# Optimization experiments

Measured on AMD Instinct MI355X. Metric: run time of the kernel, lower is better.

The kernel has to match this reference:

```python
import jax, jax.numpy as jnp
import numpy as np

# ---- single-qubit gate matrices (theta may be scalar or batched (N,)) ----

def _rx(theta):
    t = theta * 0.5
    c = jnp.cos(t).astype(jnp.complex64)
    s = jnp.sin(t).astype(jnp.complex64)
    return jnp.stack([jnp.stack([c, -1j * s], -1), jnp.stack([-1j * s, c], -1)], -2)

def _ry(theta):
    t = theta * 0.5
    c = jnp.cos(t).astype(jnp.complex64)
    s = jnp.sin(t).astype(jnp.complex64)
    return jnp.stack([jnp.stack([c, -s], -1), jnp.stack([s, c], -1)], -2)

def _rz(theta):
    t = theta * 0.5
    e = jnp.exp(-1j * t.astype(jnp.complex64))
    z = jnp.zeros_like(e)
    return jnp.stack([jnp.stack([e, z], -1), jnp.stack([z, jnp.conj(e)], -1)], -2)

def _apply_1q(state, U, wire):
    # state: (N, 2^P) complex; U: (2,2) shared or (N,2,2) per-sample
    N = state.shape[0]
    s = state.reshape(N, 2 ** wire, 2, -1)
    if U.ndim == 3:
        s = jnp.einsum('nab,nxby->nxay', U, s)
    else:
        s = jnp.einsum('ab,nxby->nxay', U, s)
    return s.reshape(N, -1)

def _apply_cnot(state, c, t, P):
    # flip target axis where control bit == 1
    N = state.shape[0]
    s = state.reshape((N,) + (2,) * P)
    ac, at = 1 + c, 1 + t
    s0 = jnp.take(s, 0, axis=ac)
    s1 = jnp.take(s, 1, axis=ac)
    at2 = at if at < ac else at - 1
    s1 = jnp.flip(s1, axis=at2)
    s = jnp.stack([s0, s1], axis=ac)
    return s.reshape(N, -1)

def _circuit(angles, qweights, P):
    # angles: (N, P, 3); qweights: (L, P, 3) -> expvals (N, P)
    N = angles.shape[0]
    state = jnp.zeros((N, 2 ** P), jnp.complex64).at[:, 0].set(1.0)
    for i in range(P):  # encoding rotations (per-sample)
        state = _apply_1q(state, _rx(angles[:, i, 0]), i)
        state = _apply_1q(state, _ry(angles[:, i, 1]), i)
        state = _apply_1q(state, _rz(angles[:, i, 2]), i)
    for L in range(qweights.shape[0]):  # variational layers (shared weights)
        for i in range(P):
            state = _apply_1q(state, _ry(qweights[L, i, 0]), i)
            state = _apply_1q(state, _rz(qweights[L, i, 1]), i)
            state = _apply_1q(state, _ry(qweights[L, i, 2]), i)
        for i in range(P):  # ring CNOTs
            state = _apply_cnot(state, i, (i + 1) % P, P)
    probs = jnp.real(state * jnp.conj(state))  # (N, 2^P)
    idx = jnp.arange(2 ** P)
    bits = (idx[None, :] >> (P - 1 - jnp.arange(P))[:, None]) & 1  # wire 0 = MSB
    signs = (1 - 2 * bits).astype(jnp.float32)  # (P, 2^P)
    return probs @ signs.T  # <Z_i> per wire, (N, P)

def setup_inputs() -> dict:
    key = jax.random.key(0)
    ks = jax.random.split(key, 6)
    B, T, P, D, L = 2, 128, 13, 64, 2
    h = jax.random.normal(ks[0], (B, T, P, D), jnp.float32)
    enc_w = jax.random.normal(ks[1], (3, D), jnp.float32) * (1.0 / np.sqrt(D))
    enc_b = jax.random.normal(ks[2], (3,), jnp.float32) * 0.1
    qweights = jax.random.normal(ks[3], (L, P, 3), jnp.float32)
    dec_w = jax.random.normal(ks[4], (D, 1), jnp.float32) * 0.1
    alpha = jnp.full((1,), 0.05, jnp.float32)
    return {"h": h, "enc_w": enc_w, "enc_b": enc_b, "qweights": qweights, "dec_w": dec_w, "alpha": alpha}

def reference(h, enc_w, enc_b, qweights, dec_w, alpha):
    B, T, P, D = h.shape
    # encoder: Linear(D, 3)
    angles = (jnp.einsum('btpd,ad->btpa', h, enc_w) + enc_b).reshape(B * T, P, 3)
    expvals = _circuit(angles, qweights, P)  # (B*T, P)
    # decoder: Linear(1, D, bias=False)
    decoded = (expvals[:, :, None] * dec_w[:, 0][None, None, :]).reshape(B, T, P, D)
    return h + alpha[0] * decoded
```

## Files before the change

### kernel.cpp

```cpp
#include <hip/hip_runtime.h>

#define P   13
#define BLK 512
#define NH  (P * 64)

typedef float2 c2;

__device__ __forceinline__ c2 cmul2(c2 a, c2 b) {
    return make_float2(a.x * b.x - a.y * b.y, a.x * b.y + a.y * b.x);
}
__device__ __forceinline__ c2 cfma2(c2 a, c2 b, c2 c) {
    return make_float2(fmaf(a.x, b.x, fmaf(-a.y, b.y, c.x)),
                       fmaf(a.x, b.y, fmaf( a.y, b.x, c.y)));
}
__device__ __forceinline__ c2 shflx2(c2 v, int m) {
    c2 r; r.x = __shfl_xor(v.x, m, 64); r.y = __shfl_xor(v.y, m, 64); return r;
}

struct RowSet { unsigned r[13]; };
constexpr RowSet chain_rows(RowSet f) {
    for (int i = 0; i < 13; ++i) { int bc = 12 - i; int bt = (i == 12) ? 12 : (11 - i); f.r[bt] ^= f.r[bc]; }
    return f;
}
constexpr RowSet chain_cols(RowSet g) {
    for (int i = 0; i < 13; ++i) { int bc = 12 - i; int bt = (i == 12) ? 12 : (11 - i); g.r[bc] ^= g.r[bt]; }
    return g;
}
constexpr RowSet R0c {{0x0C00,0x0801,0x0003,0x0006,0x000C,0x0018,0x0030,0x0060,0x00C0,0x0180,0x0300,0x1600,0x1400}};
constexpr RowSet G0c {{0x1400,0x1C00,0x1C01,0x1C03,0x1C07,0x1C0F,0x1C1F,0x1C3F,0x1C7F,0x1CFF,0x1DFF,0x1FFF,0x0FFF}};
constexpr RowSet F1c = chain_rows(R0c);
constexpr RowSet F2c = chain_rows(F1c);
constexpr RowSet G1c = chain_cols(G0c);
static_assert(G1c.r[0]==0x0400 && G1c.r[1]==0x0800 && G1c.r[2]==0x0001 && G1c.r[3]==0x0002 &&
              G1c.r[4]==0x0004 && G1c.r[5]==0x0008 && G1c.r[6]==0x0010 && G1c.r[7]==0x0020 &&
              G1c.r[8]==0x0040 && G1c.r[9]==0x0080 && G1c.r[10]==0x0100 && G1c.r[11]==0x0200 &&
              G1c.r[12]==0x1000, "single-bit gate masks after chain 1");
static_assert(F1c.r[0]==0x0400 && F1c.r[1]==0x0800 && F1c.r[2]==0x0001 && F1c.r[12]==0x1000,
              "frame after chain 1 is the bit-permutation phi");

__device__ __forceinline__ void build_V(float wa, float wb, float wc, c2* u) {
    float a = 0.5f * wa, b = 0.5f * wb, c = 0.5f * wc;
    float sa, ca, sb, cb, sc, cc;
    __sincosf(a, &sa, &ca); __sincosf(b, &sb, &cb); __sincosf(c, &sc, &cc);
    float A = ca * cb, Bq = ca * sb, C = sa * cb, D = sa * sb;
    u[0] = make_float2( cc * A - sc * C, -cc * Bq - sc * D);
    u[1] = make_float2(-cc * C - sc * A,  cc * D - sc * Bq);
    u[2] = make_float2( sc * A + cc * C, -sc * Bq + cc * D);
    u[3] = make_float2(-sc * C + cc * A,  sc * D + cc * Bq);
}

template<int K>
__device__ __forceinline__ void gate_reg(c2* s, const float* m) {
    c2 u00 = {m[0], m[1]}, u01 = {m[2], m[3]}, u10 = {m[4], m[5]}, u11 = {m[6], m[7]};
#pragma unroll
    for (int r = 0; r < 16; ++r)
        if (!(r & (1 << K))) {
            const int r1 = r | (1 << K);
            c2 a0 = s[r], a1 = s[r1];
            s[r]  = cfma2(u00, a0, cmul2(u01, a1));
            s[r1] = cfma2(u10, a0, cmul2(u11, a1));
        }
}
template<int LM>
__device__ __forceinline__ void gate_lane(c2* s, const float* m, int lane) {
    c2 u00 = {m[0], m[1]}, u01 = {m[2], m[3]}, u10 = {m[4], m[5]}, u11 = {m[6], m[7]};
    int mb = (lane & LM) ? 1 : 0;
    c2 ua = mb ? u11 : u00, ub = mb ? u10 : u01;
#pragma unroll
    for (int r = 0; r < 16; ++r) {
        c2 pv = shflx2(s[r], LM);
        s[r] = cfma2(ua, s[r], cmul2(ub, pv));
    }
}

__global__ __launch_bounds__(BLK) void qlc_kernel(
    const float* __restrict__ h, const float* __restrict__ enc_w,
    const float* __restrict__ enc_b, const float* __restrict__ qw,
    const float* __restrict__ dec_w, const float* __restrict__ alpha,
    float* __restrict__ out, int nlayers)
{
    const int n = blockIdx.x, tid = threadIdx.x, lane = tid & 63, wv = tid >> 6;
    __shared__ c2 plane[8192];
    float* smem = (float*)plane;
    float* vec  = smem;
    float* mats = smem + 64;
    c2 s[16];

    for (int p = wv; p < P; p += 8) {
        float hv = h[(size_t)n * NH + p * 64 + lane];
        float a0 = hv * enc_w[lane], a1 = hv * enc_w[64 + lane], a2 = hv * enc_w[128 + lane];
#pragma unroll
        for (int m = 32; m; m >>= 1) {
            a0 += __shfl_xor(a0, m, 64); a1 += __shfl_xor(a1, m, 64); a2 += __shfl_xor(a2, m, 64);
        }
        float x = 0.5f * (a0 + enc_b[0]), y = 0.5f * (a1 + enc_b[1]), z = 0.5f * (a2 + enc_b[2]);
        float sx, cx, sy, cy, sz, cz;
        __sincosf(x, &sx, &cx); __sincosf(y, &sy, &cy); __sincosf(z, &sz, &cz);
        c2 em = {cz, -sz}, ep = {cz, sz};
        c2 u0 = cmul2(em, make_float2(cy * cx,  sy * sx));
        c2 u1 = cmul2(ep, make_float2(sy * cx, -cy * sx));
        c2 w0 = u0, w1 = u1;
        if (nlayers > 0) {
            c2 u[4]; const float* q = qw + p * 3;
            build_V(q[0], q[1], q[2], u);
            w0 = cfma2(u[0], u0, cmul2(u[1], u1));
            w1 = cfma2(u[2], u0, cmul2(u[3], u1));
        }
        if (lane == 0) {
            int b = 12 - p;
            vec[b*4+0] = w0.x; vec[b*4+1] = w0.y; vec[b*4+2] = w1.x; vec[b*4+3] = w1.y;
        }
    }
    if (nlayers == 2 && wv == 5 && lane < P) {
        c2 u[4]; const float* q = qw + (P + lane) * 3;
        build_V(q[0], q[1], q[2], u);
        float* m = mats + lane * 8;
        m[0]=u[0].x; m[1]=u[0].y; m[2]=u[1].x; m[3]=u[1].y;
        m[4]=u[2].x; m[5]=u[2].y; m[6]=u[3].x; m[7]=u[3].y;
    }
    __syncthreads();

    {
        c2 pref = {1.f, 0.f};
        const int UB[8] = {0, 6, 7, 8, 9, 10, 11, 12};
#pragma unroll
        for (int k = 0; k < 8; ++k) {
            const int b = UB[k];
            int t = __popc(tid & (R0c.r[b] >> 4)) & 1;
            c2 vv = { vec[b*4 + t*2], vec[b*4 + t*2 + 1] };
            pref = cmul2(pref, vv);
        }
        int t1 = (tid >> 7) & 1, t5 = tid & 1;
        c2 w1v[2] = { {vec[4+t1*2], vec[5+t1*2]}, {vec[4+(t1^1)*2], vec[5+(t1^1)*2]} };
        c2 w2v[2] = { {vec[8],  vec[9]},  {vec[10], vec[11]} };
        c2 w3v[2] = { {vec[12], vec[13]}, {vec[14], vec[15]} };
        c2 w4v[2] = { {vec[16], vec[17]}, {vec[18], vec[19]} };
        c2 w5v[2] = { {vec[20+t5*2], vec[21+t5*2]}, {vec[20+(t5^1)*2], vec[21+(t5^1)*2]} };
        c2 v12[4], v34[4], P5[2];
        v12[0]=cmul2(w1v[0],w2v[0]); v12[1]=cmul2(w1v[0],w2v[1]);
        v12[2]=cmul2(w1v[1],w2v[0]); v12[3]=cmul2(w1v[1],w2v[1]);
        v34[0]=cmul2(w3v[0],w4v[0]); v34[1]=cmul2(w3v[0],w4v[1]);
        v34[2]=cmul2(w3v[1],w4v[0]); v34[3]=cmul2(w3v[1],w4v[1]);
        P5[0]=cmul2(pref,w5v[0]); P5[1]=cmul2(pref,w5v[1]);
#pragma unroll
        for (int r = 0; r < 16; ++r) {
            const int i12 = ((r & 1) << 1) | ((r ^ (r >> 1)) & 1);
            const int i34 = ((((r >> 1) ^ (r >> 2)) & 1) << 1) | (((r >> 2) ^ (r >> 3)) & 1);
            s[r] = cmul2(P5[(r >> 3) & 1], cmul2(v12[i12], v34[i34]));
        }
    }

    unsigned mrows[13];

    if (nlayers == 2) {
        gate_reg<0>(s, mats + 10*8);
        gate_reg<1>(s, mats +  9*8);
        gate_reg<2>(s, mats +  8*8);
        gate_reg<3>(s, mats +  7*8);
        gate_lane<1 >(s, mats + 6*8, lane);
        gate_lane<2 >(s, mats + 5*8, lane);
        gate_lane<4 >(s, mats + 4*8, lane);
        gate_lane<8 >(s, mats + 3*8, lane);
        gate_lane<16>(s, mats + 2*8, lane);
        gate_lane<32>(s, mats + 1*8, lane);
        c2 umA[4], umB[4], umC[4];
#pragma unroll
        for (int j = 0; j < 4; ++j) {
            umA[j] = { mats[12*8 + j*2], mats[12*8 + j*2 + 1] };
            umB[j] = { mats[11*8 + j*2], mats[11*8 + j*2 + 1] };
            umC[j] = { mats[ 0*8 + j*2], mats[ 0*8 + j*2 + 1] };
        }
        __syncthreads();
        {
            const c2* um[3] = {umA, umB, umC};
            const int  tx[3] = {64, 128, 256};
#pragma unroll
            for (int g = 0; g < 3; ++g) {
#pragma unroll
                for (int r = 0; r < 16; ++r) plane[r*512 + tid] = s[r];
                __syncthreads();
                int pt = tid ^ tx[g];
                int mb = (tid & tx[g]) ? 1 : 0;
                c2 ua = mb ? um[g][3] : um[g][0];
                c2 ub = mb ? um[g][2] : um[g][1];
#pragma unroll
                for (int r = 0; r < 16; ++r) {
                    c2 pv = plane[r*512 + pt];
                    s[r] = cfma2(ua, s[r], cmul2(ub, pv));
                }
                __syncthreads();
            }
        }
#pragma unroll
        for (int b = 0; b < 13; ++b) mrows[b] = F2c.r[b];
    } else {
        unsigned rowF[13], colG[13];
#pragma unroll
        for (int b = 0; b < 13; ++b) { rowF[b] = R0c.r[b]; colG[b] = G0c.r[b]; }
        for (int l = 1; l < nlayers; ++l) {
#pragma unroll
            for (int i = 0; i < P; ++i) { int bc = 12-i, bt = (i==12)?12:(11-i); rowF[bt]^=rowF[bc]; colG[bc]^=colG[bt]; }
#pragma unroll
            for (int b = 0; b < 13; ++b) {
                const float* q = qw + ((size_t)l * P + (12 - b)) * 3;
                c2 u[4]; build_V(q[0], q[1], q[2], u);
                __syncthreads();
#pragma unroll
                for (int r = 0; r < 16; ++r) plane[r*512 + tid] = s[r];
                __syncthreads();
                unsigned m = colG[b], row = rowF[b];
                int pt = tid ^ (int)(m >> 4);
                unsigned mr = m & 15, rl = row & 15;
                int bt_ = __popc(tid & (row >> 4)) & 1;
#pragma unroll
                for (int r = 0; r < 16; ++r) {
                    c2 pv = plane[((r ^ mr) & 15) * 512 + pt];
                    int beta = bt_ ^ (__popc(r & rl) & 1);
                    c2 ua = beta ? u[3] : u[0], ub = beta ? u[2] : u[1];
                    s[r] = cfma2(ua, s[r], cmul2(ub, pv));
                }
            }
        }
        if (nlayers >= 1) {
#pragma unroll
            for (int i = 0; i < P; ++i) { int bc = 12-i, bt = (i==12)?12:(11-i); rowF[bt]^=rowF[bc]; colG[bc]^=colG[bt]; }
        }
#pragma unroll
        for (int b = 0; b < 13; ++b) mrows[b] = rowF[b];
    }

    float pr[16];
#pragma unroll
    for (int r = 0; r < 16; ++r) pr[r] = fmaf(s[r].x, s[r].x, s[r].y * s[r].y);
    float ev[13];
#pragma unroll
    for (int b = 0; b < 13; ++b) {
        unsigned row = mrows[b];
        int tp = __popc(tid & (row >> 4)) & 1;
        float acc = 0.f;
#pragma unroll
        for (int r = 0; r < 16; ++r)
            acc += (__popc((unsigned)r & row) & 1) ? -pr[r] : pr[r];
        ev[12 - b] = tp ? -acc : acc;
    }
#pragma unroll
    for (int w = 0; w < 13; ++w) {
#pragma unroll
        for (int m = 32; m; m >>= 1) ev[w] += __shfl_xor(ev[w], m, 64);
    }
    float* red  = smem + 256;
    float* red2 = smem + 384;
    __syncthreads();
    if (lane == 0) {
#pragma unroll
        for (int w = 0; w < 13; ++w) red[wv * 13 + w] = ev[w];
    }
    __syncthreads();
    if (tid < 13) {
        float sum = 0.f;
        for (int q = 0; q < 8; ++q) sum += red[q * 13 + tid];
        red2[tid] = sum;
    }
    __syncthreads();
    float al = alpha[0];
    for (int idx = tid; idx < NH; idx += BLK) {
        size_t off = (size_t)n * NH + idx;
        out[off] = fmaf(al * red2[idx >> 6], dec_w[idx & 63], h[off]);
    }
}

extern "C" void kernel_launch(void* const* d_in, const int* in_sizes, int n_in,
                              void* d_out, int out_size, void* d_ws, size_t ws_size,
                              hipStream_t stream) {
    const float* h     = (const float*)d_in[0];
    const float* enc_w = (const float*)d_in[1];
    const float* enc_b = (const float*)d_in[2];
    const float* qw    = (const float*)d_in[3];
    const float* dec_w = (const float*)d_in[4];
    const float* alpha = (const float*)d_in[5];
    float* out = (float*)d_out;

    int N = in_sizes[0] / NH;
    int L = in_sizes[3] / (P * 3);

    qlc_kernel<<<N, BLK, 0, stream>>>(h, enc_w, enc_b, qw, dec_w, alpha, out, L);
}
```

Baseline: 81.16 us.

## Fuse pairs of lane/shared-memory gates into 4x4 ops and prefetch h for output

Pairs of single-qubit gates on lane-mapped wires are combined into one Kronecker-product 4x4 update. That cuts six shuffle-gate passes to three, each doing three shuffles. The two shared-memory gates on thread bits 64 and 128 are merged into one exchange, removing one write/sync/read round trip through LDS. The h values, dec_w and alpha for the final residual write are loaded at kernel start, so the global reads overlap the quantum simulation. This raises shuffle and LDS read counts per pass and register pressure in exchange for fewer passes and barriers.

```diff
diff --git a/kernel.cpp b/kernel.cpp
--- a/kernel.cpp
+++ b/kernel.cpp
@@ -61,15 +61,24 @@
             s[r1] = cfma2(u10, a0, cmul2(u11, a1));
         }
 }
-template<int LM>
-__device__ __forceinline__ void gate_lane(c2* s, const float* m, int lane) {
-    c2 u00 = {m[0], m[1]}, u01 = {m[2], m[3]}, u10 = {m[4], m[5]}, u11 = {m[6], m[7]};
-    int mb = (lane & LM) ? 1 : 0;
-    c2 ua = mb ? u11 : u00, ub = mb ? u10 : u01;
+
+template<int M1, int M2>
+__device__ __forceinline__ void gate_lane2(c2* s, const float* mU, const float* mV, int lane) {
+    c2 u00={mU[0],mU[1]}, u01={mU[2],mU[3]}, u10={mU[4],mU[5]}, u11={mU[6],mU[7]};
+    c2 v00={mV[0],mV[1]}, v01={mV[2],mV[3]}, v10={mV[4],mV[5]}, v11={mV[6],mV[7]};
+    int a = (lane & M1) ? 1 : 0, b = (lane & M2) ? 1 : 0;
+    c2 Ud = a ? u11 : u00, Uo = a ? u10 : u01;
+    c2 Vd = b ? v11 : v00, Vo = b ? v10 : v01;
+    c2 wS = cmul2(Ud, Vd), w1 = cmul2(Uo, Vd), w2 = cmul2(Ud, Vo), w3 = cmul2(Uo, Vo);
 #pragma unroll
     for (int r = 0; r < 16; ++r) {
-        c2 pv = shflx2(s[r], LM);
-        s[r] = cfma2(ua, s[r], cmul2(ub, pv));
+        c2 p1 = shflx2(s[r], M1);
+        c2 p2 = shflx2(s[r], M2);
+        c2 p3 = shflx2(s[r], M1 | M2);
+        c2 t = cmul2(wS, s[r]);
+        t = cfma2(w1, p1, t);
+        t = cfma2(w2, p2, t);
+        s[r] = cfma2(w3, p3, t);
     }
 }
 
@@ -86,8 +95,14 @@
     float* mats = smem + 64;
     c2 s[16];
 
+    const size_t rowoff = (size_t)n * NH;
+    float h0 = h[rowoff + tid];
+    float h1 = (tid < NH - 512) ? h[rowoff + 512 + tid] : 0.f;
+    float dw = dec_w[tid & 63];
+    float al = alpha[0];
+
     for (int p = wv; p < P; p += 8) {
-        float hv = h[(size_t)n * NH + p * 64 + lane];
+        float hv = h[rowoff + p * 64 + lane];
         float a0 = hv * enc_w[lane], a1 = hv * enc_w[64 + lane], a2 = hv * enc_w[128 + lane];
 #pragma unroll
         for (int m = 32; m; m >>= 1) {
@@ -157,12 +172,9 @@
         gate_reg<1>(s, mats +  9*8);
         gate_reg<2>(s, mats +  8*8);
         gate_reg<3>(s, mats +  7*8);
-        gate_lane<1 >(s, mats + 6*8, lane);
-        gate_lane<2 >(s, mats + 5*8, lane);
-        gate_lane<4 >(s, mats + 4*8, lane);
-        gate_lane<8 >(s, mats + 3*8, lane);
-        gate_lane<16>(s, mats + 2*8, lane);
-        gate_lane<32>(s, mats + 1*8, lane);
+        gate_lane2<1,  2>(s, mats + 6*8, mats + 5*8, lane);
+        gate_lane2<4,  8>(s, mats + 4*8, mats + 3*8, lane);
+        gate_lane2<16,32>(s, mats + 2*8, mats + 1*8, lane);
         c2 umA[4], umB[4], umC[4];
 #pragma unroll
         for (int j = 0; j < 4; ++j) {
@@ -171,24 +183,38 @@
             umC[j] = { mats[ 0*8 + j*2], mats[ 0*8 + j*2 + 1] };
         }
         __syncthreads();
+#pragma unroll
+        for (int r = 0; r < 16; ++r) plane[r*512 + tid] = s[r];
+        __syncthreads();
         {
-            const c2* um[3] = {umA, umB, umC};
-            const int  tx[3] = {64, 128, 256};
-#pragma unroll
-            for (int g = 0; g < 3; ++g) {
-#pragma unroll
-                for (int r = 0; r < 16; ++r) plane[r*512 + tid] = s[r];
-                __syncthreads();
-                int pt = tid ^ tx[g];
-                int mb = (tid & tx[g]) ? 1 : 0;
-                c2 ua = mb ? um[g][3] : um[g][0];
-                c2 ub = mb ? um[g][2] : um[g][1];
-#pragma unroll
-                for (int r = 0; r < 16; ++r) {
-                    c2 pv = plane[r*512 + pt];
-                    s[r] = cfma2(ua, s[r], cmul2(ub, pv));
-                }
-                __syncthreads();
+            int a = (tid >> 6) & 1, b = (tid >> 7) & 1;
+            c2 Ud = a ? umA[3] : umA[0], Uo = a ? umA[2] : umA[1];
+            c2 Vd = b ? umB[3] : umB[0], Vo = b ? umB[2] : umB[1];
+            c2 wS = cmul2(Ud, Vd), w1 = cmul2(Uo, Vd), w2 = cmul2(Ud, Vo), w3 = cmul2(Uo, Vo);
+            int p1 = tid ^ 64, p2 = tid ^ 128, p3 = tid ^ 192;
+#pragma unroll
+            for (int r = 0; r < 16; ++r) {
+                c2 a1 = plane[r*512 + p1];
+                c2 a2 = plane[r*512 + p2];
+                c2 a3 = plane[r*512 + p3];
+                c2 t = cmul2(wS, s[r]);
+                t = cfma2(w1, a1, t);
+                t = cfma2(w2, a2, t);
+                s[r] = cfma2(w3, a3, t);
+            }
+        }
+        __syncthreads();
+#pragma unroll
+        for (int r = 0; r < 16; ++r) plane[r*512 + tid] = s[r];
+        __syncthreads();
+        {
+            int mb = (tid >> 8) & 1;
+            c2 ua = mb ? umC[3] : umC[0], ub = mb ? umC[2] : umC[1];
+            int pt = tid ^ 256;
+#pragma unroll
+            for (int r = 0; r < 16; ++r) {
+                c2 pv = plane[r*512 + pt];
+                s[r] = cfma2(ua, s[r], cmul2(ub, pv));
             }
         }
 #pragma unroll
@@ -262,11 +288,9 @@
         red2[tid] = sum;
     }
     __syncthreads();
-    float al = alpha[0];
-    for (int idx = tid; idx < NH; idx += BLK) {
-        size_t off = (size_t)n * NH + idx;
-        out[off] = fmaf(al * red2[idx >> 6], dec_w[idx & 63], h[off]);
-    }
+    out[rowoff + tid] = fmaf(al * red2[wv], dw, h0);
+    if (tid < NH - 512)
+        out[rowoff + 512 + tid] = fmaf(al * red2[wv + 8], dw, h1);
 }
 
 extern "C" void kernel_launch(void* const* d_in, const int* in_sizes, int n_in,
```

Result: slower. 86.32 us (+6.4%).
